# Kernel optimization log

Hardware: AMD Instinct MI355X
Metric: run time of the kernel (lower is better)

## Reference

```python
import jax, jax.numpy as jnp
import numpy as np

H = 128; TIME_DIM = 8; LAM = 0.01; NUM_LAYERS = 2; B = 64
N_FACT = 100000; N_COMP = 5000; E = 500000; D_FACT = 384; D_COMP = 64
MLP_IN = 2 + 2 * (TIME_DIM // 2) + 1  # 11


def setup_inputs() -> dict:
    key = jax.random.key(0)
    ks = jax.random.split(key, 40)
    rn = lambda k, sh, s=0.05: jax.random.normal(k, sh, jnp.float32) * s
    inp = {
        'x_fact': jax.random.normal(ks[0], (N_FACT, D_FACT), jnp.float32),
        'x_comp': jax.random.normal(ks[1], (N_COMP, D_COMP), jnp.float32),
        'ea_f2c': jax.random.uniform(ks[2], (E, 2), jnp.float32),
        'ea_c2f': jax.random.uniform(ks[3], (E, 2), jnp.float32),
        'ei_f2c_src': jax.random.randint(ks[4], (E,), 0, N_FACT, jnp.int32),
        'ei_f2c_dst': jax.random.randint(ks[5], (E,), 0, N_COMP, jnp.int32),
        'ei_c2f_src': jax.random.randint(ks[6], (E,), 0, N_COMP, jnp.int32),
        'ei_c2f_dst': jax.random.randint(ks[7], (E,), 0, N_FACT, jnp.int32),
        'fact_batch': jnp.sort(jax.random.randint(ks[8], (N_FACT,), 0, B, jnp.int32)),
        'comp_batch': jnp.sort(jax.random.randint(ks[9], (N_COMP,), 0, B, jnp.int32)),
        # lazy per-type input projections
        'W_in_fact': rn(ks[10], (D_FACT, H)), 'b_in_fact': jnp.zeros((H,), jnp.float32),
        'W_in_comp': rn(ks[11], (D_COMP, H)), 'b_in_comp': jnp.zeros((H,), jnp.float32),
        # EdgeAttrEncoder MLP: 11 -> 32 -> 16 -> 1
        'eW1': rn(ks[12], (MLP_IN, 32)), 'eb1': jnp.zeros((32,), jnp.float32),
        'eW2': rn(ks[13], (32, 16)), 'eb2': jnp.zeros((16,), jnp.float32),
        'eW3': rn(ks[14], (16, 1)), 'eb3': jnp.zeros((1,), jnp.float32),
        # GraphConv per layer (axis0) per edge type (axis1: 0=f->c, 1=c->f)
        'W_rel': rn(ks[15], (NUM_LAYERS, 2, H, H)), 'b_rel': jnp.zeros((NUM_LAYERS, 2, H), jnp.float32),
        'W_root': rn(ks[16], (NUM_LAYERS, 2, H, H)),
        # shared post LayerNorm per node type (axis0: 0=fact, 1=company)
        'ln_scale': jnp.ones((2, H), jnp.float32), 'ln_bias': jnp.zeros((2, H), jnp.float32),
        # classifier 2H -> H -> 1
        'Wc1': rn(ks[17], (2 * H, H)), 'bc1': jnp.zeros((H,), jnp.float32),
        'Wc2': rn(ks[18], (H, 1)), 'bc2': jnp.zeros((1,), jnp.float32),
    }
    return inp


def _edge_gate(ea, eW1, eb1, eW2, eb2, eW3, eb3):
    # ea: [E,2] -> gate [E]
    sent = jnp.clip(ea[:, 0:1], -1.0, 1.0)
    decay = ea[:, 1:2]
    # decay in [0,1] -> delta_t = -log(decay)/lambda, clamped >= 0
    dt = jnp.maximum(-jnp.log(jnp.clip(decay, 1e-6, None)) / LAM, 0.0)
    ds = jnp.clip(dt / 30.0, 0.0, 12.0)
    freqs = jnp.arange(1, TIME_DIM // 2 + 1, dtype=ds.dtype)
    tvec = jnp.concatenate([jnp.sin(ds * freqs), jnp.cos(ds * freqs), ds], axis=-1)
    x = jnp.concatenate([sent, jnp.log1p(dt), tvec], axis=-1)  # [E,11]
    h = jax.nn.relu(x @ eW1 + eb1)
    h = jax.nn.relu(h @ eW2 + eb2)
    return jax.nn.sigmoid(h @ eW3 + eb3)[:, 0]


def _layernorm(x, scale, bias, eps=1e-5):
    mu = jnp.mean(x, axis=-1, keepdims=True)
    var = jnp.var(x, axis=-1, keepdims=True)
    return (x - mu) * jax.lax.rsqrt(var + eps) * scale + bias


def _seg_mean(x, seg, n):
    s = jax.ops.segment_sum(x, seg, num_segments=n)
    c = jax.ops.segment_sum(jnp.ones((x.shape[0], 1), x.dtype), seg, num_segments=n)
    return s / jnp.maximum(c, 1.0)


def reference(x_fact, x_comp, ea_f2c, ea_c2f, ei_f2c_src, ei_f2c_dst, ei_c2f_src,
              ei_c2f_dst, fact_batch, comp_batch, W_in_fact, b_in_fact, W_in_comp,
              b_in_comp, eW1, eb1, eW2, eb2, eW3, eb3, W_rel, b_rel, W_root,
              ln_scale, ln_bias, Wc1, bc1, Wc2, bc2):
    # per-type input projection + ReLU
    xf = jax.nn.relu(x_fact @ W_in_fact + b_in_fact)   # [N_fact, H]
    xc = jax.nn.relu(x_comp @ W_in_comp + b_in_comp)   # [N_comp, H]
    # MLP-gated edge weights (shared encoder across relations)
    w_f2c = _edge_gate(ea_f2c, eW1, eb1, eW2, eb2, eW3, eb3)  # [E]
    w_c2f = _edge_gate(ea_c2f, eW1, eb1, eW2, eb2, eW3, eb3)  # [E]
    nf, nc = xf.shape[0], xc.shape[0]
    for l in range(NUM_LAYERS):
        prev_f, prev_c = xf, xc
        # GraphConv: lin_rel(sum_j w_ij * x_j) + lin_root(x_i)  (aggr='add')
        agg_c = jax.ops.segment_sum(xf[ei_f2c_src] * w_f2c[:, None], ei_f2c_dst, num_segments=nc)
        new_c = agg_c @ W_rel[l, 0] + b_rel[l, 0] + xc @ W_root[l, 0]
        agg_f = jax.ops.segment_sum(xc[ei_c2f_src] * w_c2f[:, None], ei_c2f_dst, num_segments=nf)
        new_f = agg_f @ W_rel[l, 1] + b_rel[l, 1] + xf @ W_root[l, 1]
        # ReLU -> residual -> shared per-type LayerNorm
        xf = _layernorm(jax.nn.relu(new_f) + prev_f, ln_scale[0], ln_bias[0])
        xc = _layernorm(jax.nn.relu(new_c) + prev_c, ln_scale[1], ln_bias[1])
    fact_pool = _seg_mean(xf, fact_batch, B)   # [B, H]
    comp_pool = _seg_mean(xc, comp_batch, B)   # [B, H]
    pooled = jnp.concatenate([fact_pool, comp_pool], axis=-1)  # [B, 2H]
    h = jax.nn.relu(pooled @ Wc1 + bc1)
    return (h @ Wc2 + bc2)[:, 0]  # [B] logits
```

## Files before the change

### kernel.cpp

```cpp
#include <hip/hip_runtime.h>
#include <math.h>

#define H 128
#define EDGES 500000
#define NFACT 100000
#define NCOMP 5000
#define BATCH 64
#define NTILE 6250

typedef _Float16 half8_t __attribute__((ext_vector_type(8)));
typedef float floatx4 __attribute__((ext_vector_type(4)));

__device__ inline short4 f4_to_h4(float4 v){
  union { short4 s; _Float16 h[4]; } u;
  u.h[0]=(_Float16)v.x; u.h[1]=(_Float16)v.y; u.h[2]=(_Float16)v.z; u.h[3]=(_Float16)v.w;
  return u.s;
}

__global__ __launch_bounds__(1024) void k_scan1(const int* __restrict__ cnt, int n,
                                                int* __restrict__ offs, int* __restrict__ part){
  __shared__ int sh[1024];
  int tid = threadIdx.x;
  int i = blockIdx.x*1024 + tid;
  int v = (i < n) ? cnt[i] : 0;
  sh[tid] = v;
  __syncthreads();
  for (int d = 1; d < 1024; d <<= 1){
    int t = (tid >= d) ? sh[tid-d] : 0;
    __syncthreads();
    sh[tid] += t;
    __syncthreads();
  }
  if (i < n) offs[i] = sh[tid] - v;
  if (tid == 1023) part[blockIdx.x] = sh[1023];
}

__global__ void k_scan2(int* part, int nb){
  __shared__ int sh[128];
  int tid = threadIdx.x;
  int v = (tid < nb) ? part[tid] : 0;
  sh[tid] = v;
  __syncthreads();
  for (int d = 1; d < 128; d <<= 1){
    int t = (tid >= d) ? sh[tid-d] : 0;
    __syncthreads();
    sh[tid] += t;
    __syncthreads();
  }
  if (tid < nb) part[tid] = sh[tid] - v;
}

__global__ __launch_bounds__(1024) void k_scan3(int* offs, int n, const int* __restrict__ part, int total){
  int i = blockIdx.x*1024 + threadIdx.x;
  if (i < n) offs[i] += part[blockIdx.x];
  if (i == 0) offs[n] = total;
}

__global__ void k_fill2d(const int* __restrict__ src0, const int* __restrict__ dst0,
                         const float* __restrict__ w0, const int* __restrict__ offs0,
                         int* __restrict__ cur0, int4* __restrict__ ed0,
                         const int* __restrict__ src1, const int* __restrict__ dst1,
                         const float* __restrict__ w1, const int* __restrict__ offs1,
                         int* __restrict__ cur1, int4* __restrict__ ed1, int n){
  int half = gridDim.x >> 1;
  int dir = blockIdx.x >= half;
  const int* src = dir ? src1 : src0;
  const int* dst = dir ? dst1 : dst0;
  const float* w = dir ? w1 : w0;
  const int* offs = dir ? offs1 : offs0;
  int* cur = dir ? cur1 : cur0;
  int4* ed = dir ? ed1 : ed0;
  int bid = blockIdx.x - (dir ? half : 0);
  for (int e = bid*blockDim.x + threadIdx.x; e < n; e += half*blockDim.x){
    int d = dst[e];
    int p = offs[d] + atomicAdd(&cur[d], 1);
    ed[p] = make_int4(src[e], __float_as_int(w[e]), d, 0);
  }
}

__global__ __launch_bounds__(256) void k_prep(const float* __restrict__ W_in,
                                              const float* __restrict__ W_rel,
                                              const float* __restrict__ W_root,
                                              _Float16* __restrict__ wt_in,
                                              _Float16* __restrict__ wcat0,
                                              _Float16* __restrict__ wcat1){
  int i = blockIdx.x*256 + threadIdx.x;
  if (i < 49152){
    int n = i / 384, k = i % 384;
    wt_in[i] = (_Float16)W_in[k*128 + n];
  } else if (i < 49152 + 32768){
    int j = i - 49152;
    int n = j / 256, k = j % 256;
    const float* Wr = W_rel  + 1*16384;
    const float* Wo = W_root + 1*16384;
    wcat0[j] = (_Float16)(k < 128 ? Wr[k*128+n] : Wo[(k-128)*128+n]);
  } else if (i < 49152 + 65536){
    int j = i - 49152 - 32768;
    int n = j / 256, k = j % 256;
    const float* Wr = W_rel  + 3*16384;
    const float* Wo = W_root + 3*16384;
    wcat1[j] = (_Float16)(k < 128 ? Wr[k*128+n] : Wo[(k-128)*128+n]);
  }
}

__global__ __launch_bounds__(256) void k_gate2(const float* __restrict__ ea0,
                       const float* __restrict__ ea1,
                       const int* __restrict__ dst0, const int* __restrict__ dst1,
                       int* __restrict__ cnt0, int* __restrict__ cnt1,
                       const float* __restrict__ eW1, const float* __restrict__ eb1,
                       const float* __restrict__ eW2, const float* __restrict__ eb2,
                       const float* __restrict__ eW3, const float* __restrict__ eb3,
                       float* __restrict__ wout0, float* __restrict__ wout1, int n){
  __shared__ float w1t[32*12];
  __shared__ float w2s[32*16];
  __shared__ float b1s[32], b2s[16], w3s[16];
  __shared__ float b3s;
  int tid = threadIdx.x;
  for (int i = tid; i < 352; i += 256){
    int k = i >> 5, c = i & 31;
    w1t[c*12 + k] = eW1[i];
  }
  if (tid < 32) w1t[tid*12 + 11] = 0.f;
  for (int i = tid; i < 512; i += 256) w2s[i] = eW2[i];
  if (tid < 32) b1s[tid] = eb1[tid];
  if (tid < 16) b2s[tid] = eb2[tid];
  if (tid < 16) w3s[tid] = eW3[tid];
  if (tid == 0) b3s = eb3[0];
  __syncthreads();

  int half = gridDim.x >> 1;
  int dir = blockIdx.x >= half;
  const float* ea = dir ? ea1 : ea0;
  const int* dst  = dir ? dst1 : dst0;
  int* cnt        = dir ? cnt1 : cnt0;
  float* wout     = dir ? wout1 : wout0;
  int bid = blockIdx.x - (dir ? half : 0);

  const float4* w1t4 = (const float4*)w1t;
  const float4* w24  = (const float4*)w2s;
  float4 b2v0 = ((const float4*)b2s)[0], b2v1 = ((const float4*)b2s)[1];
  float4 b2v2 = ((const float4*)b2s)[2], b2v3 = ((const float4*)b2s)[3];
  float4 w3v0 = ((const float4*)w3s)[0], w3v1 = ((const float4*)w3s)[1];
  float4 w3v2 = ((const float4*)w3s)[2], w3v3 = ((const float4*)w3s)[3];

  for (int e = bid*blockDim.x + tid; e < n; e += half*blockDim.x){
    float2 eav = ((const float2*)ea)[e];
    float sent  = fminf(fmaxf(eav.x, -1.f), 1.f);
    float decay = eav.y;
    float dt = fmaxf(-__logf(fmaxf(decay, 1e-6f)) * 100.f, 0.f);
    float ds = fminf(dt * (1.f/30.f), 12.f);
    float s1 = __sinf(ds), c1 = __cosf(ds);
    float s2v = 2.f*s1*c1;
    float c2v = 1.f - 2.f*s1*s1;
    float s3v = s1*c2v + c1*s2v;
    float c3v = c1*c2v - s1*s2v;
    float s4v = 2.f*s2v*c2v;
    float c4v = 1.f - 2.f*s2v*s2v;
    float4 x0 = make_float4(sent, __logf(1.f + dt), s1, s2v);
    float4 x1 = make_float4(s3v, s4v, c1, c2v);
    float4 x2 = make_float4(c3v, c4v, ds, 0.f);

    float4 sa = b2v0, sb = b2v1, sc = b2v2, sd = b2v3;
    #pragma unroll 2
    for (int i = 0; i < 32; i++){
      float4 wa = w1t4[i*3+0], wb = w1t4[i*3+1], wc = w1t4[i*3+2];
      float h = b1s[i];
      h += x0.x*wa.x + x0.y*wa.y + x0.z*wa.z + x0.w*wa.w;
      h += x1.x*wb.x + x1.y*wb.y + x1.z*wb.z + x1.w*wb.w;
      h += x2.x*wc.x + x2.y*wc.y + x2.z*wc.z;
      h = fmaxf(h, 0.f);
      float4 va = w24[i*4+0], vb = w24[i*4+1], vc = w24[i*4+2], vd = w24[i*4+3];
      sa.x += h*va.x; sa.y += h*va.y; sa.z += h*va.z; sa.w += h*va.w;
      sb.x += h*vb.x; sb.y += h*vb.y; sb.z += h*vb.z; sb.w += h*vb.w;
      sc.x += h*vc.x; sc.y += h*vc.y; sc.z += h*vc.z; sc.w += h*vc.w;
      sd.x += h*vd.x; sd.y += h*vd.y; sd.z += h*vd.z; sd.w += h*vd.w;
    }
    float o = b3s;
    o += fmaxf(sa.x,0.f)*w3v0.x + fmaxf(sa.y,0.f)*w3v0.y + fmaxf(sa.z,0.f)*w3v0.z + fmaxf(sa.w,0.f)*w3v0.w;
    o += fmaxf(sb.x,0.f)*w3v1.x + fmaxf(sb.y,0.f)*w3v1.y + fmaxf(sb.z,0.f)*w3v1.z + fmaxf(sb.w,0.f)*w3v1.w;
    o += fmaxf(sc.x,0.f)*w3v2.x + fmaxf(sc.y,0.f)*w3v2.y + fmaxf(sc.z,0.f)*w3v2.z + fmaxf(sc.w,0.f)*w3v2.w;
    o += fmaxf(sd.x,0.f)*w3v3.x + fmaxf(sd.y,0.f)*w3v3.y + fmaxf(sd.z,0.f)*w3v3.z + fmaxf(sd.w,0.f)*w3v3.w;
    wout[e] = __fdividef(1.f, 1.f + __expf(-o));
    atomicAdd(&cnt[dst[e]], 1);
  }
}

template<int K, int R>
__global__ __launch_bounds__(128) void k_input_s(const float* __restrict__ X, const float* __restrict__ W,
                                                 const float* __restrict__ bias, float* __restrict__ Y){
  __shared__ float xs[R*K];
  int t = threadIdx.x;
  long row0 = (long)blockIdx.x * R;
  const float4* src = (const float4*)(X + row0*K);
  float4* d4 = (float4*)xs;
  for (int i = t; i < R*K/4; i += 128) d4[i] = src[i];
  __syncthreads();
  float acc[R];
  #pragma unroll
  for (int r = 0; r < R; r++) acc[r] = 0.f;
  for (int k4 = 0; k4 < K/4; k4++){
    int kb = k4*4;
    float w0 = W[(kb+0)*H+t], w1 = W[(kb+1)*H+t], w2 = W[(kb+2)*H+t], w3 = W[(kb+3)*H+t];
    #pragma unroll
    for (int r = 0; r < R; r++){
      float4 xv = ((const float4*)(xs + r*K))[k4];
      acc[r] += xv.x*w0 + xv.y*w1 + xv.z*w2 + xv.w*w3;
    }
  }
  float b = bias[t];
  #pragma unroll
  for (int r = 0; r < R; r++)
    Y[(row0+r)*H + t] = fmaxf(acc[r] + b, 0.f);
}

__global__ __launch_bounds__(256, 2) void k_input_m(const float* __restrict__ X,
                                                 const _Float16* __restrict__ Wt,
                                                 const float* __restrict__ bias,
                                                 float* __restrict__ Y){
  __shared__ _Float16 xs[16][392];
  __shared__ float tb[4*16*36];
  int t = threadIdx.x;
  int lane = t & 63, wv = t >> 6;
  int m = lane & 15, q = lane >> 4;

  half8_t wreg[2][12];
  float bcol[2];
  #pragma unroll
  for (int j = 0; j < 2; j++){
    int col = (wv*2 + j)*16 + m;
    const _Float16* wb = Wt + (size_t)col*384 + q*8;
    #pragma unroll
    for (int ks = 0; ks < 12; ks++) wreg[j][ks] = *(const half8_t*)(wb + ks*32);
    bcol[j] = bias[col];
  }

  int row_i[6], c4_i[6];
  #pragma unroll
  for (int i = 0; i < 6; i++){
    int idx = i*256 + t;
    row_i[i] = idx/96; c4_i[i] = idx - row_i[i]*96;
  }

  int tpb = (NTILE + gridDim.x - 1)/gridDim.x;
  int tb0 = blockIdx.x*tpb, tb1 = tb0 + tpb;
  if (tb1 > NTILE) tb1 = NTILE;
  if (tb0 >= tb1) return;

  const float4* X4 = (const float4*)X;
  float4 r[6];
  #pragma unroll
  for (int i = 0; i < 6; i++) r[i] = X4[(size_t)tb0*1536 + i*256 + t];

  float* tbw = &tb[wv*576];
  int rowl = lane >> 2, c8l = lane & 3;

  for (int tile = tb0; tile < tb1; ++tile){
    __syncthreads();
    #pragma unroll
    for (int i = 0; i < 6; i++)
      *(short4*)&xs[row_i[i]][c4_i[i]*4] = f4_to_h4(r[i]);
    __syncthreads();
    if (tile + 1 < tb1){
      size_t base = (size_t)(tile+1)*1536;
      #pragma unroll
      for (int i = 0; i < 6; i++) r[i] = X4[base + i*256 + t];
    }
    __builtin_amdgcn_sched_barrier(0);

    floatx4 acc0 = (floatx4){0.f,0.f,0.f,0.f};
    floatx4 acc1 = (floatx4){0.f,0.f,0.f,0.f};
    #pragma unroll
    for (int ks = 0; ks < 12; ks++){
      half8_t av = *(const half8_t*)&xs[m][ks*32 + q*8];
      acc0 = __builtin_amdgcn_mfma_f32_16x16x32_f16(av, wreg[0][ks], acc0, 0, 0, 0);
      acc1 = __builtin_amdgcn_mfma_f32_16x16x32_f16(av, wreg[1][ks], acc1, 0, 0, 0);
    }
    long rb = (long)tile*16;
    #pragma unroll
    for (int j = 0; j < 2; j++){
      floatx4 a = j ? acc1 : acc0;
      int lc = j*16 + m;
      #pragma unroll
      for (int i2 = 0; i2 < 4; i2++)
        tbw[(q*4+i2)*36 + lc] = fmaxf(a[i2] + bcol[j], 0.f);
    }
    __syncthreads();
    {
      const float* srcp = tbw + rowl*36 + c8l*8;
      float* dstp = Y + (rb + rowl)*H + wv*32 + c8l*8;
      *(float4*)dstp       = *(const float4*)(srcp);
      *(float4*)(dstp + 4) = *(const float4*)(srcp + 4);
    }
  }
}

__global__ __launch_bounds__(256) void k_layer_m(
    const float* __restrict__ xsrc, const float* __restrict__ xprev,
    const int* __restrict__ offs, const int4* __restrict__ ed,
    const _Float16* __restrict__ Wt, const float* __restrict__ brel,
    const float* __restrict__ lnsc, const float* __restrict__ lnbi,
    float* __restrict__ xnext){
  __shared__ float tball[4*2304];
  int t = threadIdx.x;
  int lane = t & 63, wv = t >> 6;
  long tile = (long)blockIdx.x*4 + wv;
  if (tile*16 >= NFACT) return;
  long row0 = tile*16;
  float* tb = tball + wv*2304;
  _Float16 (*xin)[264] = reinterpret_cast<_Float16 (*)[264]>(tb);
  int c = lane & 31, g = lane >> 5;
  int grow0 = g*8;
  #pragma unroll
  for (int j = 0; j < 8; j++){
    int lr = grow0 + j;
    ((short4*)&xin[lr][0])[c] = make_short4(0,0,0,0);
    float4 pv = ((const float4*)(xprev + (row0+lr)*H))[c];
    ((short4*)&xin[lr][128])[c] = f4_to_h4(pv);
  }
  int lo = offs[row0 + grow0], hi = offs[row0 + grow0 + 8];
  float4 a = make_float4(0.f,0.f,0.f,0.f);
  int cur = (int)row0 + grow0;
  int idx = lo;
  int nb = (hi - lo) >> 3;
  int4 rec[8];
  if (nb > 0){
    #pragma unroll
    for (int j = 0; j < 8; j++) rec[j] = ed[idx+j];
  }
  for (int b = 0; b < nb; b++){
    int nxt = idx + 8;
    int4 rec2[8];
    if (b + 1 < nb){
      #pragma unroll
      for (int j = 0; j < 8; j++) rec2[j] = ed[nxt+j];
    }
    float4 v[8];
    #pragma unroll
    for (int j = 0; j < 8; j++) v[j] = ((const float4*)(xsrc + (long)rec[j].x*H))[c];
    #pragma unroll
    for (int j = 0; j < 8; j++){
      float w = __int_as_float(rec[j].y);
      if (rec[j].z != cur){ ((short4*)&xin[cur-(int)row0][0])[c] = f4_to_h4(a); a = make_float4(0.f,0.f,0.f,0.f); cur = rec[j].z; }
      a.x += v[j].x*w; a.y += v[j].y*w; a.z += v[j].z*w; a.w += v[j].w*w;
    }
    #pragma unroll
    for (int j = 0; j < 8; j++) rec[j] = rec2[j];
    idx = nxt;
  }
  for (; idx < hi; idx++){
    int4 mrec = ed[idx];
    float4 v = ((const float4*)(xsrc + (long)mrec.x*H))[c];
    float w = __int_as_float(mrec.y);
    if (mrec.z != cur){ ((short4*)&xin[cur-(int)row0][0])[c] = f4_to_h4(a); a = make_float4(0.f,0.f,0.f,0.f); cur = mrec.z; }
    a.x += v.x*w; a.y += v.y*w; a.z += v.z*w; a.w += v.w*w;
  }
  if (lo < hi) ((short4*)&xin[cur-(int)row0][0])[c] = f4_to_h4(a);

  int m = lane & 15, q = lane >> 4;
  floatx4 acc[8];
  #pragma unroll
  for (int nt = 0; nt < 8; nt++) acc[nt] = (floatx4){0.f,0.f,0.f,0.f};
  #pragma unroll
  for (int ks = 0; ks < 8; ks++){
    half8_t av = *(const half8_t*)&xin[m][ks*32 + q*8];
    #pragma unroll
    for (int nt = 0; nt < 8; nt++){
      half8_t bv = *(const half8_t*)(Wt + (size_t)(nt*16 + m)*256 + ks*32 + q*8);
      acc[nt] = __builtin_amdgcn_mfma_f32_16x16x32_f16(av, bv, acc[nt], 0, 0, 0);
    }
  }
  float vs[8][4];
  float s[4] = {0.f,0.f,0.f,0.f}, ss[4] = {0.f,0.f,0.f,0.f};
  #pragma unroll
  for (int nt = 0; nt < 8; nt++){
    int col = nt*16 + m;
    float b = brel[col];
    #pragma unroll
    for (int i = 0; i < 4; i++){
      int lr = q*4 + i;
      float pv = (float)xin[lr][128 + col];
      float v = fmaxf(acc[nt][i] + b, 0.f) + pv;
      vs[nt][i] = v;
      s[i] += v; ss[i] += v*v;
    }
  }
  #pragma unroll
  for (int i = 0; i < 4; i++){
    #pragma unroll
    for (int mm = 1; mm < 16; mm <<= 1){
      s[i]  += __shfl_xor(s[i],  mm, 64);
      ss[i] += __shfl_xor(ss[i], mm, 64);
    }
  }
  asm volatile("" ::: "memory");
  #pragma unroll
  for (int nt = 0; nt < 8; nt++){
    int col = nt*16 + m;
    float lsc = lnsc[col], lbi = lnbi[col];
    int chnk = col >> 5, lc = col & 31;
    #pragma unroll
    for (int i = 0; i < 4; i++){
      float mu  = s[i]*(1.f/H);
      float var = ss[i]*(1.f/H) - mu*mu;
      float rstd = rsqrtf(var + 1e-5f);
      tb[(q*4+i)*144 + chnk*36 + lc] = (vs[nt][i] - mu)*rstd*lsc + lbi;
    }
  }
  asm volatile("" ::: "memory");
  {
    int rowl = lane >> 2, c8 = lane & 3;
    const float* srcp = &tb[rowl*144 + c8*36];
    float4* dst4 = (float4*)(xnext + (row0 + rowl)*H + c8*32);
    #pragma unroll
    for (int k = 0; k < 8; k++)
      dst4[k] = *(const float4*)(srcp + k*4);
  }
}

template<int R>
__global__ __launch_bounds__(128) void k_layer(
    const float* __restrict__ xsrc, const float* __restrict__ xprev,
    const int* __restrict__ offs, const int4* __restrict__ ed,
    const float* __restrict__ Wrel, const float* __restrict__ brel,
    const float* __restrict__ Wroot, const float* __restrict__ lnsc,
    const float* __restrict__ lnbi, float* __restrict__ xnext){
  constexpr int RG = R/4;
  __shared__ float xin[R][256];
  int t = threadIdx.x, c = t & 31, g = t >> 5;
  long row0 = (long)blockIdx.x * R;
  int grow0 = g*RG;
  #pragma unroll
  for (int j = 0; j < RG; j++){
    int lr = grow0 + j;
    ((float4*)&xin[lr][0])[c] = make_float4(0.f,0.f,0.f,0.f);
    ((float4*)&xin[lr][128])[c] = ((const float4*)(xprev + (row0+lr)*H))[c];
  }
  int lo = offs[row0 + grow0], hi = offs[row0 + grow0 + RG];
  float4 a = make_float4(0.f,0.f,0.f,0.f);
  int cur = (int)row0 + grow0;
  int idx = lo;
  for (; idx + 8 <= hi; idx += 8){
    int4 m[8];
    #pragma unroll
    for (int j = 0; j < 8; j++) m[j] = ed[idx+j];
    float4 v[8];
    #pragma unroll
    for (int j = 0; j < 8; j++) v[j] = ((const float4*)(xsrc + (long)m[j].x*H))[c];
    #pragma unroll
    for (int j = 0; j < 8; j++){
      float w = __int_as_float(m[j].y);
      if (m[j].z != cur){ ((float4*)&xin[cur-(int)row0][0])[c] = a; a = make_float4(0.f,0.f,0.f,0.f); cur = m[j].z; }
      a.x += v[j].x*w; a.y += v[j].y*w; a.z += v[j].z*w; a.w += v[j].w*w;
    }
  }
  for (; idx < hi; idx++){
    int4 m = ed[idx];
    float4 v = ((const float4*)(xsrc + (long)m.x*H))[c];
    float w = __int_as_float(m.y);
    if (m.z != cur){ ((float4*)&xin[cur-(int)row0][0])[c] = a; a = make_float4(0.f,0.f,0.f,0.f); cur = m.z; }
    a.x += v.x*w; a.y += v.y*w; a.z += v.z*w; a.w += v.w*w;
  }
  if (lo < hi) ((float4*)&xin[cur-(int)row0][0])[c] = a;

  float4 acc[RG];
  float4 bv = ((const float4*)brel)[c];
  #pragma unroll
  for (int j = 0; j < RG; j++) acc[j] = bv;
  #pragma unroll
  for (int p = 0; p < 2; p++){
    const float4* Wp = (const float4*)(p ? Wroot : Wrel) + c;
    #pragma unroll 4
    for (int k4 = 0; k4 < 32; k4++){
      float4 xv[RG];
      #pragma unroll
      for (int j = 0; j < RG; j++)
        xv[j] = ((const float4*)xin[grow0+j])[p*32 + k4];
      #pragma unroll
      for (int kk = 0; kk < 4; kk++){
        float4 wv = Wp[(size_t)(k4*4+kk)*32];
        #pragma unroll
        for (int j = 0; j < RG; j++){
          float xk = (kk==0) ? xv[j].x : (kk==1) ? xv[j].y : (kk==2) ? xv[j].z : xv[j].w;
          acc[j].x += xk*wv.x; acc[j].y += xk*wv.y; acc[j].z += xk*wv.z; acc[j].w += xk*wv.w;
        }
      }
    }
  }
  float4 lsc = ((const float4*)lnsc)[c];
  float4 lbi = ((const float4*)lnbi)[c];
  #pragma unroll
  for (int j = 0; j < RG; j++){
    int lr = grow0 + j;
    float4 pv = ((const float4*)&xin[lr][128])[c];
    float4 v;
    v.x = fmaxf(acc[j].x, 0.f) + pv.x;
    v.y = fmaxf(acc[j].y, 0.f) + pv.y;
    v.z = fmaxf(acc[j].z, 0.f) + pv.z;
    v.w = fmaxf(acc[j].w, 0.f) + pv.w;
    float s  = v.x + v.y + v.z + v.w;
    float ss = v.x*v.x + v.y*v.y + v.z*v.z + v.w*v.w;
    #pragma unroll
    for (int mm = 1; mm < 32; mm <<= 1){ s += __shfl_xor(s, mm, 64); ss += __shfl_xor(ss, mm, 64); }
    float mu  = s*(1.f/H);
    float var = ss*(1.f/H) - mu*mu;
    float rstd = rsqrtf(var + 1e-5f);
    float4 o;
    o.x = (v.x - mu)*rstd*lsc.x + lbi.x;
    o.y = (v.y - mu)*rstd*lsc.y + lbi.y;
    o.z = (v.z - mu)*rstd*lsc.z + lbi.z;
    o.w = (v.w - mu)*rstd*lsc.w + lbi.w;
    ((float4*)(xnext + (row0+lr)*H))[c] = o;
  }
}

#define PCHUNK 128
#define FBLK ((NFACT + PCHUNK - 1) / PCHUNK)
#define CBLK ((NCOMP + PCHUNK - 1) / PCHUNK)

__global__ __launch_bounds__(128) void k_pool_acc(const float* __restrict__ xf, const float* __restrict__ xc,
                                                  const int* __restrict__ fb, const int* __restrict__ cb,
                                                  float* __restrict__ pooled){
  int t = threadIdx.x;
  int b = blockIdx.x;
  if (b < FBLK){
    int start = b*PCHUNK, end = start + PCHUNK; if (end > NFACT) end = NFACT;
    float s = 0.f; int curb = -1;
    for (int i = start; i < end; i++){
      int bb = fb[i];
      if (bb != curb){
        if (curb >= 0) atomicAdd(&pooled[curb*256 + t], s);
        curb = bb; s = 0.f;
      }
      s += xf[(long)i*H + t];
    }
    if (curb >= 0) atomicAdd(&pooled[curb*256 + t], s);
  } else {
    int bbk = b - FBLK;
    int start = bbk*PCHUNK, end = start + PCHUNK; if (end > NCOMP) end = NCOMP;
    float s = 0.f; int curb = -1;
    for (int i = start; i < end; i++){
      int bb = cb[i];
      if (bb != curb){
        if (curb >= 0) atomicAdd(&pooled[curb*256 + 128 + t], s);
        curb = bb; s = 0.f;
      }
      s += xc[(long)i*H + t];
    }
    if (curb >= 0) atomicAdd(&pooled[curb*256 + 128 + t], s);
  }
}

__device__ inline int lowerb(const int* a, int n, int key){
  int lo = 0, hi = n;
  while (lo < hi){ int m = (lo+hi) >> 1; if (a[m] < key) lo = m+1; else hi = m; }
  return lo;
}

__global__ __launch_bounds__(128) void k_head(const float* __restrict__ pooled,
                                              const int* __restrict__ fb, const int* __restrict__ cb,
                                              const float* __restrict__ Wc1, const float* __restrict__ bc1,
                                              const float* __restrict__ Wc2, const float* __restrict__ bc2,
                                              float* __restrict__ out){
  __shared__ float p[256];
  __shared__ float red[2];
  int t = threadIdx.x, b = blockIdx.x;
  int flo = lowerb(fb, NFACT, b), fhi = lowerb(fb, NFACT, b+1);
  int clo = lowerb(cb, NCOMP, b), chi = lowerb(cb, NCOMP, b+1);
  float fc = (float)((fhi - flo) > 1 ? (fhi - flo) : 1);
  float cc = (float)((chi - clo) > 1 ? (chi - clo) : 1);
  p[t]       = pooled[b*256 + t] / fc;
  p[128 + t] = pooled[b*256 + 128 + t] / cc;
  __syncthreads();
  float acc = bc1[t];
  #pragma unroll 4
  for (int k = 0; k < 256; k++) acc += p[k]*Wc1[k*H + t];
  float h = fmaxf(acc, 0.f)*Wc2[t];
  #pragma unroll
  for (int m = 1; m < 64; m <<= 1) h += __shfl_xor(h, m, 64);
  if ((t & 63) == 0) red[t>>6] = h;
  __syncthreads();
  if (t == 0) out[b] = red[0] + red[1] + bc2[0];
}

extern "C" void kernel_launch(void* const* d_in, const int* in_sizes, int n_in,
                              void* d_out, int out_size, void* d_ws, size_t ws_size,
                              hipStream_t stream){
  const float* x_fact = (const float*)d_in[0];
  const float* x_comp = (const float*)d_in[1];
  const float* ea_f2c = (const float*)d_in[2];
  const float* ea_c2f = (const float*)d_in[3];
  const int* s_f2c   = (const int*)d_in[4];
  const int* dst_f2c = (const int*)d_in[5];
  const int* s_c2f   = (const int*)d_in[6];
  const int* dst_c2f = (const int*)d_in[7];
  const int* fb = (const int*)d_in[8];
  const int* cb = (const int*)d_in[9];
  const float* W_in_f = (const float*)d_in[10];
  const float* b_in_f = (const float*)d_in[11];
  const float* W_in_c = (const float*)d_in[12];
  const float* b_in_c = (const float*)d_in[13];
  const float* eW1 = (const float*)d_in[14]; const float* eb1 = (const float*)d_in[15];
  const float* eW2 = (const float*)d_in[16]; const float* eb2 = (const float*)d_in[17];
  const float* eW3 = (const float*)d_in[18]; const float* eb3 = (const float*)d_in[19];
  const float* W_rel = (const float*)d_in[20]; const float* b_rel = (const float*)d_in[21];
  const float* W_root = (const float*)d_in[22];
  const float* ln_s = (const float*)d_in[23]; const float* ln_b = (const float*)d_in[24];
  const float* Wc1 = (const float*)d_in[25]; const float* bc1 = (const float*)d_in[26];
  const float* Wc2 = (const float*)d_in[27]; const float* bc2 = (const float*)d_in[28];
  float* out = (float*)d_out;

  char* ws = (char*)d_ws;
  size_t off = 0;
  auto alloc = [&](size_t bytes)->char*{ char* p = ws + off; off = (off + bytes + 255) & ~(size_t)255; return p; };
  float* xf0   = (float*)alloc((size_t)NFACT*H*4);
  float* xf1   = (float*)alloc((size_t)NFACT*H*4);
  float* xc0   = (float*)alloc((size_t)NCOMP*H*4);
  float* xc1   = (float*)alloc((size_t)NCOMP*H*4);
  float* w_f2c = (float*)alloc((size_t)EDGES*4);
  float* w_c2f = (float*)alloc((size_t)EDGES*4);
  int4* ed_f2c = (int4*)alloc((size_t)EDGES*16);
  int4* ed_c2f = (int4*)alloc((size_t)EDGES*16);
  int* off_f2c = (int*)alloc((size_t)(NCOMP+1)*4);
  int* cur_f2c = (int*)alloc((size_t)NCOMP*4);
  int* off_c2f = (int*)alloc((size_t)(NFACT+1)*4);
  int* cur_c2f = (int*)alloc((size_t)NFACT*4);
  int* part    = (int*)alloc(128*4);
  float* pooled= (float*)alloc((size_t)BATCH*256*4);
  _Float16* wt_in = (_Float16*)alloc((size_t)49152*2);
  _Float16* wcat0 = (_Float16*)alloc((size_t)32768*2);
  _Float16* wcat1 = (_Float16*)alloc((size_t)32768*2);

  k_prep<<<448,256,0,stream>>>(W_in_f, W_rel, W_root, wt_in, wcat0, wcat1);
  hipMemsetAsync(cur_f2c, 0, NCOMP*4, stream);
  hipMemsetAsync(cur_c2f, 0, NFACT*4, stream);
  k_gate2<<<1024,256,0,stream>>>(ea_f2c, ea_c2f, dst_f2c, dst_c2f,
                                 cur_f2c, cur_c2f,
                                 eW1,eb1,eW2,eb2,eW3,eb3, w_f2c, w_c2f, EDGES);

  {
    int nb = (NCOMP + 1023)/1024;
    k_scan1<<<nb,1024,0,stream>>>(cur_f2c, NCOMP, off_f2c, part);
    k_scan2<<<1,128,0,stream>>>(part, nb);
    k_scan3<<<nb,1024,0,stream>>>(off_f2c, NCOMP, part, EDGES);
  }
  {
    int nb = (NFACT + 1023)/1024;
    k_scan1<<<nb,1024,0,stream>>>(cur_c2f, NFACT, off_c2f, part);
    k_scan2<<<1,128,0,stream>>>(part, nb);
    k_scan3<<<nb,1024,0,stream>>>(off_c2f, NFACT, part, EDGES);
  }
  hipMemsetAsync(cur_f2c, 0, NCOMP*4, stream);
  hipMemsetAsync(cur_c2f, 0, NFACT*4, stream);
  k_fill2d<<<1024,256,0,stream>>>(s_f2c, dst_f2c, w_f2c, off_f2c, cur_f2c, ed_f2c,
                                  s_c2f, dst_c2f, w_c2f, off_c2f, cur_c2f, ed_c2f, EDGES);

  k_input_m<<<512,256,0,stream>>>(x_fact, wt_in, b_in_f, xf0);
  k_input_s<64,8><<<NCOMP/8,128,0,stream>>>(x_comp, W_in_c, b_in_c, xc0);

  const float* xf_p = xf0; const float* xc_p = xc0;
  float* xf_n = xf1; float* xc_n = xc1;
  for (int l = 0; l < 2; l++){
    const float* Wr0 = W_rel  + (size_t)(l*2+0)*H*H;
    const float* br0 = b_rel  + (size_t)(l*2+0)*H;
    const float* br1 = b_rel  + (size_t)(l*2+1)*H;
    const float* Wo0 = W_root + (size_t)(l*2+0)*H*H;
    const _Float16* wcat = (l == 0) ? wcat0 : wcat1;
    k_layer<4><<<NCOMP/4,128,0,stream>>>(xf_p, xc_p, off_f2c, ed_f2c,
                                         Wr0, br0, Wo0, ln_s + H, ln_b + H, xc_n);
    k_layer_m<<<(NTILE+3)/4,256,0,stream>>>(xc_p, xf_p, off_c2f, ed_c2f,
                                            wcat, br1, ln_s, ln_b, xf_n);
    const float* tf = xf_p; xf_p = xf_n; xf_n = (float*)tf;
    const float* tc = xc_p; xc_p = xc_n; xc_n = (float*)tc;
  }

  hipMemsetAsync(pooled, 0, (size_t)BATCH*256*4, stream);
  k_pool_acc<<<FBLK + CBLK,128,0,stream>>>(xf_p, xc_p, fb, cb, pooled);
  k_head<<<BATCH,128,0,stream>>>(pooled, fb, cb, Wc1, bc1, Wc2, bc2, out);
}
```

Measured before the change: 803.6 us.

## Fuse company and fact GraphConv layer kernels into one launch

Replaces the two per-layer kernels (company update and fact update) with a single launch. Block index selects the branch: the first blocks run the MFMA fact path and the rest run the scalar company path, two 4-row tiles per 256-thread block. Since both updates read only the previous layer's state, the latency-bound company gathers (about 100 edges per row) can overlap with the fact work instead of running serially, and one launch is saved per layer. In exchange, every block now reserves the larger shared-memory buffer, and the fact branch loses its software prefetch of the next batch of edge records, which may raise gather latency.

```diff
diff --git a/kernel.cpp b/kernel.cpp
--- a/kernel.cpp
+++ b/kernel.cpp
@@ -7,6 +7,8 @@
 #define NCOMP 5000
 #define BATCH 64
 #define NTILE 6250
+#define NFB 1563
+#define NCB 625
 
 typedef _Float16 half8_t __attribute__((ext_vector_type(8)));
 typedef float floatx4 __attribute__((ext_vector_type(4)));
@@ -294,222 +296,196 @@
   }
 }
 
-__global__ __launch_bounds__(256) void k_layer_m(
-    const float* __restrict__ xsrc, const float* __restrict__ xprev,
-    const int* __restrict__ offs, const int4* __restrict__ ed,
-    const _Float16* __restrict__ Wt, const float* __restrict__ brel,
-    const float* __restrict__ lnsc, const float* __restrict__ lnbi,
-    float* __restrict__ xnext){
-  __shared__ float tball[4*2304];
+__global__ __launch_bounds__(256) void k_layer_fused(
+    const float* __restrict__ xf_p, const float* __restrict__ xc_p,
+    const int* __restrict__ offs_c, const int4* __restrict__ ed_c,
+    const float* __restrict__ Wrel, const float* __restrict__ brc,
+    const float* __restrict__ Wroot,
+    const float* __restrict__ lnsC, const float* __restrict__ lnbC,
+    float* __restrict__ xc_n,
+    const int* __restrict__ offs_f, const int4* __restrict__ ed_f,
+    const _Float16* __restrict__ Wt, const float* __restrict__ brf,
+    const float* __restrict__ lnsF, const float* __restrict__ lnbF,
+    float* __restrict__ xf_n){
+  __shared__ __align__(16) float smemf[9216];
   int t = threadIdx.x;
-  int lane = t & 63, wv = t >> 6;
-  long tile = (long)blockIdx.x*4 + wv;
-  if (tile*16 >= NFACT) return;
-  long row0 = tile*16;
-  float* tb = tball + wv*2304;
-  _Float16 (*xin)[264] = reinterpret_cast<_Float16 (*)[264]>(tb);
-  int c = lane & 31, g = lane >> 5;
-  int grow0 = g*8;
-  #pragma unroll
-  for (int j = 0; j < 8; j++){
-    int lr = grow0 + j;
-    ((short4*)&xin[lr][0])[c] = make_short4(0,0,0,0);
-    float4 pv = ((const float4*)(xprev + (row0+lr)*H))[c];
-    ((short4*)&xin[lr][128])[c] = f4_to_h4(pv);
-  }
-  int lo = offs[row0 + grow0], hi = offs[row0 + grow0 + 8];
-  float4 a = make_float4(0.f,0.f,0.f,0.f);
-  int cur = (int)row0 + grow0;
-  int idx = lo;
-  int nb = (hi - lo) >> 3;
-  int4 rec[8];
-  if (nb > 0){
-    #pragma unroll
-    for (int j = 0; j < 8; j++) rec[j] = ed[idx+j];
-  }
-  for (int b = 0; b < nb; b++){
-    int nxt = idx + 8;
-    int4 rec2[8];
-    if (b + 1 < nb){
-      #pragma unroll
-      for (int j = 0; j < 8; j++) rec2[j] = ed[nxt+j];
-    }
-    float4 v[8];
-    #pragma unroll
-    for (int j = 0; j < 8; j++) v[j] = ((const float4*)(xsrc + (long)rec[j].x*H))[c];
+  if ((int)blockIdx.x < NFB){
+    int lane = t & 63, wv = t >> 6;
+    long tile = (long)blockIdx.x*4 + wv;
+    if (tile >= NTILE) return;
+    long row0 = tile*16;
+    float* tb = smemf + wv*2304;
+    _Float16 (*xin)[264] = reinterpret_cast<_Float16 (*)[264]>(tb);
+    int c = lane & 31, g = lane >> 5;
+    int grow0 = g*8;
     #pragma unroll
     for (int j = 0; j < 8; j++){
-      float w = __int_as_float(rec[j].y);
-      if (rec[j].z != cur){ ((short4*)&xin[cur-(int)row0][0])[c] = f4_to_h4(a); a = make_float4(0.f,0.f,0.f,0.f); cur = rec[j].z; }
-      a.x += v[j].x*w; a.y += v[j].y*w; a.z += v[j].z*w; a.w += v[j].w*w;
-    }
-    #pragma unroll
-    for (int j = 0; j < 8; j++) rec[j] = rec2[j];
-    idx = nxt;
-  }
-  for (; idx < hi; idx++){
-    int4 mrec = ed[idx];
-    float4 v = ((const float4*)(xsrc + (long)mrec.x*H))[c];
-    float w = __int_as_float(mrec.y);
-    if (mrec.z != cur){ ((short4*)&xin[cur-(int)row0][0])[c] = f4_to_h4(a); a = make_float4(0.f,0.f,0.f,0.f); cur = mrec.z; }
-    a.x += v.x*w; a.y += v.y*w; a.z += v.z*w; a.w += v.w*w;
-  }
-  if (lo < hi) ((short4*)&xin[cur-(int)row0][0])[c] = f4_to_h4(a);
-
-  int m = lane & 15, q = lane >> 4;
-  floatx4 acc[8];
-  #pragma unroll
-  for (int nt = 0; nt < 8; nt++) acc[nt] = (floatx4){0.f,0.f,0.f,0.f};
-  #pragma unroll
-  for (int ks = 0; ks < 8; ks++){
-    half8_t av = *(const half8_t*)&xin[m][ks*32 + q*8];
+      int lr = grow0 + j;
+      ((short4*)&xin[lr][0])[c] = make_short4(0,0,0,0);
+      float4 pv = ((const float4*)(xf_p + (row0+lr)*H))[c];
+      ((short4*)&xin[lr][128])[c] = f4_to_h4(pv);
+    }
+    int lo = offs_f[row0 + grow0], hi = offs_f[row0 + grow0 + 8];
+    float4 a = make_float4(0.f,0.f,0.f,0.f);
+    int cur = (int)row0 + grow0;
+    int idx = lo;
+    for (; idx + 8 <= hi; idx += 8){
+      int4 rec[8];
+      #pragma unroll
+      for (int j = 0; j < 8; j++) rec[j] = ed_f[idx+j];
+      float4 v[8];
+      #pragma unroll
+      for (int j = 0; j < 8; j++) v[j] = ((const float4*)(xc_p + (long)rec[j].x*H))[c];
+      #pragma unroll
+      for (int j = 0; j < 8; j++){
+        float w = __int_as_float(rec[j].y);
+        if (rec[j].z != cur){ ((short4*)&xin[cur-(int)row0][0])[c] = f4_to_h4(a); a = make_float4(0.f,0.f,0.f,0.f); cur = rec[j].z; }
+        a.x += v[j].x*w; a.y += v[j].y*w; a.z += v[j].z*w; a.w += v[j].w*w;
+      }
+    }
+    for (; idx < hi; idx++){
+      int4 rec = ed_f[idx];
+      float4 v = ((const float4*)(xc_p + (long)rec.x*H))[c];
+      float w = __int_as_float(rec.y);
+      if (rec.z != cur){ ((short4*)&xin[cur-(int)row0][0])[c] = f4_to_h4(a); a = make_float4(0.f,0.f,0.f,0.f); cur = rec.z; }
+      a.x += v.x*w; a.y += v.y*w; a.z += v.z*w; a.w += v.w*w;
+    }
+    if (lo < hi) ((short4*)&xin[cur-(int)row0][0])[c] = f4_to_h4(a);
+
+    int m = lane & 15, q = lane >> 4;
+    floatx4 acc[8];
+    #pragma unroll
+    for (int nt = 0; nt < 8; nt++) acc[nt] = (floatx4){0.f,0.f,0.f,0.f};
+    #pragma unroll
+    for (int ks = 0; ks < 8; ks++){
+      half8_t av = *(const half8_t*)&xin[m][ks*32 + q*8];
+      #pragma unroll
+      for (int nt = 0; nt < 8; nt++){
+        half8_t bv = *(const half8_t*)(Wt + (size_t)(nt*16 + m)*256 + ks*32 + q*8);
+        acc[nt] = __builtin_amdgcn_mfma_f32_16x16x32_f16(av, bv, acc[nt], 0, 0, 0);
+      }
+    }
+    float vs[8][4];
+    float s[4] = {0.f,0.f,0.f,0.f}, ss[4] = {0.f,0.f,0.f,0.f};
     #pragma unroll
     for (int nt = 0; nt < 8; nt++){
-      half8_t bv = *(const half8_t*)(Wt + (size_t)(nt*16 + m)*256 + ks*32 + q*8);
-      acc[nt] = __builtin_amdgcn_mfma_f32_16x16x32_f16(av, bv, acc[nt], 0, 0, 0);
-    }
-  }
-  float vs[8][4];
-  float s[4] = {0.f,0.f,0.f,0.f}, ss[4] = {0.f,0.f,0.f,0.f};
-  #pragma unroll
-  for (int nt = 0; nt < 8; nt++){
-    int col = nt*16 + m;
-    float b = brel[col];
+      int col = nt*16 + m;
+      float b = brf[col];
+      #pragma unroll
+      for (int i = 0; i < 4; i++){
+        int lr = q*4 + i;
+        float pv = (float)xin[lr][128 + col];
+        float v = fmaxf(acc[nt][i] + b, 0.f) + pv;
+        vs[nt][i] = v;
+        s[i] += v; ss[i] += v*v;
+      }
+    }
     #pragma unroll
     for (int i = 0; i < 4; i++){
-      int lr = q*4 + i;
-      float pv = (float)xin[lr][128 + col];
-      float v = fmaxf(acc[nt][i] + b, 0.f) + pv;
-      vs[nt][i] = v;
-      s[i] += v; ss[i] += v*v;
-    }
-  }
-  #pragma unroll
-  for (int i = 0; i < 4; i++){
-    #pragma unroll
-    for (int mm = 1; mm < 16; mm <<= 1){
-      s[i]  += __shfl_xor(s[i],  mm, 64);
-      ss[i] += __shfl_xor(ss[i], mm, 64);
-    }
-  }
-  asm volatile("" ::: "memory");
-  #pragma unroll
-  for (int nt = 0; nt < 8; nt++){
-    int col = nt*16 + m;
-    float lsc = lnsc[col], lbi = lnbi[col];
-    int chnk = col >> 5, lc = col & 31;
-    #pragma unroll
-    for (int i = 0; i < 4; i++){
-      float mu  = s[i]*(1.f/H);
-      float var = ss[i]*(1.f/H) - mu*mu;
+      #pragma unroll
+      for (int mm = 1; mm < 16; mm <<= 1){
+        s[i]  += __shfl_xor(s[i],  mm, 64);
+        ss[i] += __shfl_xor(ss[i], mm, 64);
+      }
+    }
+    asm volatile("" ::: "memory");
+    #pragma unroll
+    for (int nt = 0; nt < 8; nt++){
+      int col = nt*16 + m;
+      float lsc = lnsF[col], lbi = lnbF[col];
+      int chnk = col >> 5, lc = col & 31;
+      #pragma unroll
+      for (int i = 0; i < 4; i++){
+        float mu  = s[i]*(1.f/H);
+        float var = ss[i]*(1.f/H) - mu*mu;
+        float rstd = rsqrtf(var + 1e-5f);
+        tb[(q*4+i)*144 + chnk*36 + lc] = (vs[nt][i] - mu)*rstd*lsc + lbi;
+      }
+    }
+    asm volatile("" ::: "memory");
+    {
+      int rowl = lane >> 2, c8 = lane & 3;
+      const float* srcp = &tb[rowl*144 + c8*36];
+      float4* dst4 = (float4*)(xf_n + (row0 + rowl)*H + c8*32);
+      #pragma unroll
+      for (int k = 0; k < 8; k++)
+        dst4[k] = *(const float4*)(srcp + k*4);
+    }
+  } else {
+    int unit = t >> 7, tt = t & 127;
+    int ctile = ((int)blockIdx.x - NFB)*2 + unit;
+    float (*xin)[256] = (float(*)[256])(smemf + unit*1024);
+    int c = tt & 31, g = tt >> 5;
+    long row0 = (long)ctile * 4;
+    {
+      ((float4*)&xin[g][0])[c] = make_float4(0.f,0.f,0.f,0.f);
+      ((float4*)&xin[g][128])[c] = ((const float4*)(xc_p + (row0+g)*H))[c];
+    }
+    int lo = offs_c[row0 + g], hi = offs_c[row0 + g + 1];
+    float4 a = make_float4(0.f,0.f,0.f,0.f);
+    int cur = (int)row0 + g;
+    int idx = lo;
+    for (; idx + 8 <= hi; idx += 8){
+      int4 rec[8];
+      #pragma unroll
+      for (int j = 0; j < 8; j++) rec[j] = ed_c[idx+j];
+      float4 v[8];
+      #pragma unroll
+      for (int j = 0; j < 8; j++) v[j] = ((const float4*)(xf_p + (long)rec[j].x*H))[c];
+      #pragma unroll
+      for (int j = 0; j < 8; j++){
+        float w = __int_as_float(rec[j].y);
+        if (rec[j].z != cur){ ((float4*)&xin[cur-(int)row0][0])[c] = a; a = make_float4(0.f,0.f,0.f,0.f); cur = rec[j].z; }
+        a.x += v[j].x*w; a.y += v[j].y*w; a.z += v[j].z*w; a.w += v[j].w*w;
+      }
+    }
+    for (; idx < hi; idx++){
+      int4 rec = ed_c[idx];
+      float4 v = ((const float4*)(xf_p + (long)rec.x*H))[c];
+      float w = __int_as_float(rec.y);
+      if (rec.z != cur){ ((float4*)&xin[cur-(int)row0][0])[c] = a; a = make_float4(0.f,0.f,0.f,0.f); cur = rec.z; }
+      a.x += v.x*w; a.y += v.y*w; a.z += v.z*w; a.w += v.w*w;
+    }
+    if (lo < hi) ((float4*)&xin[cur-(int)row0][0])[c] = a;
+
+    float4 acc = ((const float4*)brc)[c];
+    #pragma unroll
+    for (int p = 0; p < 2; p++){
+      const float4* Wp = (const float4*)(p ? Wroot : Wrel) + c;
+      #pragma unroll 4
+      for (int k4 = 0; k4 < 32; k4++){
+        float4 xv = ((const float4*)xin[g])[p*32 + k4];
+        #pragma unroll
+        for (int kk = 0; kk < 4; kk++){
+          float4 wv = Wp[(size_t)(k4*4+kk)*32];
+          float xk = (kk==0) ? xv.x : (kk==1) ? xv.y : (kk==2) ? xv.z : xv.w;
+          acc.x += xk*wv.x; acc.y += xk*wv.y; acc.z += xk*wv.z; acc.w += xk*wv.w;
+        }
+      }
+    }
+    float4 lsc = ((const float4*)lnsC)[c];
+    float4 lbi = ((const float4*)lnbC)[c];
+    {
+      float4 pv = ((const float4*)&xin[g][128])[c];
+      float4 v;
+      v.x = fmaxf(acc.x, 0.f) + pv.x;
+      v.y = fmaxf(acc.y, 0.f) + pv.y;
+      v.z = fmaxf(acc.z, 0.f) + pv.z;
+      v.w = fmaxf(acc.w, 0.f) + pv.w;
+      float s  = v.x + v.y + v.z + v.w;
+      float ss = v.x*v.x + v.y*v.y + v.z*v.z + v.w*v.w;
+      #pragma unroll
+      for (int mm = 1; mm < 32; mm <<= 1){ s += __shfl_xor(s, mm, 64); ss += __shfl_xor(ss, mm, 64); }
+      float mu  = s*(1.f/H);
+      float var = ss*(1.f/H) - mu*mu;
       float rstd = rsqrtf(var + 1e-5f);
-      tb[(q*4+i)*144 + chnk*36 + lc] = (vs[nt][i] - mu)*rstd*lsc + lbi;
-    }
-  }
-  asm volatile("" ::: "memory");
-  {
-    int rowl = lane >> 2, c8 = lane & 3;
-    const float* srcp = &tb[rowl*144 + c8*36];
-    float4* dst4 = (float4*)(xnext + (row0 + rowl)*H + c8*32);
-    #pragma unroll
-    for (int k = 0; k < 8; k++)
-      dst4[k] = *(const float4*)(srcp + k*4);
-  }
-}
-
-template<int R>
-__global__ __launch_bounds__(128) void k_layer(
-    const float* __restrict__ xsrc, const float* __restrict__ xprev,
-    const int* __restrict__ offs, const int4* __restrict__ ed,
-    const float* __restrict__ Wrel, const float* __restrict__ brel,
-    const float* __restrict__ Wroot, const float* __restrict__ lnsc,
-    const float* __restrict__ lnbi, float* __restrict__ xnext){
-  constexpr int RG = R/4;
-  __shared__ float xin[R][256];
-  int t = threadIdx.x, c = t & 31, g = t >> 5;
-  long row0 = (long)blockIdx.x * R;
-  int grow0 = g*RG;
-  #pragma unroll
-  for (int j = 0; j < RG; j++){
-    int lr = grow0 + j;
-    ((float4*)&xin[lr][0])[c] = make_float4(0.f,0.f,0.f,0.f);
-    ((float4*)&xin[lr][128])[c] = ((const float4*)(xprev + (row0+lr)*H))[c];
-  }
-  int lo = offs[row0 + grow0], hi = offs[row0 + grow0 + RG];
-  float4 a = make_float4(0.f,0.f,0.f,0.f);
-  int cur = (int)row0 + grow0;
-  int idx = lo;
-  for (; idx + 8 <= hi; idx += 8){
-    int4 m[8];
-    #pragma unroll
-    for (int j = 0; j < 8; j++) m[j] = ed[idx+j];
-    float4 v[8];
-    #pragma unroll
-    for (int j = 0; j < 8; j++) v[j] = ((const float4*)(xsrc + (long)m[j].x*H))[c];
-    #pragma unroll
-    for (int j = 0; j < 8; j++){
-      float w = __int_as_float(m[j].y);
-      if (m[j].z != cur){ ((float4*)&xin[cur-(int)row0][0])[c] = a; a = make_float4(0.f,0.f,0.f,0.f); cur = m[j].z; }
-      a.x += v[j].x*w; a.y += v[j].y*w; a.z += v[j].z*w; a.w += v[j].w*w;
-    }
-  }
-  for (; idx < hi; idx++){
-    int4 m = ed[idx];
-    float4 v = ((const float4*)(xsrc + (long)m.x*H))[c];
-    float w = __int_as_float(m.y);
-    if (m.z != cur){ ((float4*)&xin[cur-(int)row0][0])[c] = a; a = make_float4(0.f,0.f,0.f,0.f); cur = m.z; }
-    a.x += v.x*w; a.y += v.y*w; a.z += v.z*w; a.w += v.w*w;
-  }
-  if (lo < hi) ((float4*)&xin[cur-(int)row0][0])[c] = a;
-
-  float4 acc[RG];
-  float4 bv = ((const float4*)brel)[c];
-  #pragma unroll
-  for (int j = 0; j < RG; j++) acc[j] = bv;
-  #pragma unroll
-  for (int p = 0; p < 2; p++){
-    const float4* Wp = (const float4*)(p ? Wroot : Wrel) + c;
-    #pragma unroll 4
-    for (int k4 = 0; k4 < 32; k4++){
-      float4 xv[RG];
-      #pragma unroll
-      for (int j = 0; j < RG; j++)
-        xv[j] = ((const float4*)xin[grow0+j])[p*32 + k4];
-      #pragma unroll
-      for (int kk = 0; kk < 4; kk++){
-        float4 wv = Wp[(size_t)(k4*4+kk)*32];
-        #pragma unroll
-        for (int j = 0; j < RG; j++){
-          float xk = (kk==0) ? xv[j].x : (kk==1) ? xv[j].y : (kk==2) ? xv[j].z : xv[j].w;
-          acc[j].x += xk*wv.x; acc[j].y += xk*wv.y; acc[j].z += xk*wv.z; acc[j].w += xk*wv.w;
-        }
-      }
-    }
-  }
-  float4 lsc = ((const float4*)lnsc)[c];
-  float4 lbi = ((const float4*)lnbi)[c];
-  #pragma unroll
-  for (int j = 0; j < RG; j++){
-    int lr = grow0 + j;
-    float4 pv = ((const float4*)&xin[lr][128])[c];
-    float4 v;
-    v.x = fmaxf(acc[j].x, 0.f) + pv.x;
-    v.y = fmaxf(acc[j].y, 0.f) + pv.y;
-    v.z = fmaxf(acc[j].z, 0.f) + pv.z;
-    v.w = fmaxf(acc[j].w, 0.f) + pv.w;
-    float s  = v.x + v.y + v.z + v.w;
-    float ss = v.x*v.x + v.y*v.y + v.z*v.z + v.w*v.w;
-    #pragma unroll
-    for (int mm = 1; mm < 32; mm <<= 1){ s += __shfl_xor(s, mm, 64); ss += __shfl_xor(ss, mm, 64); }
-    float mu  = s*(1.f/H);
-    float var = ss*(1.f/H) - mu*mu;
-    float rstd = rsqrtf(var + 1e-5f);
-    float4 o;
-    o.x = (v.x - mu)*rstd*lsc.x + lbi.x;
-    o.y = (v.y - mu)*rstd*lsc.y + lbi.y;
-    o.z = (v.z - mu)*rstd*lsc.z + lbi.z;
-    o.w = (v.w - mu)*rstd*lsc.w + lbi.w;
-    ((float4*)(xnext + (row0+lr)*H))[c] = o;
+      float4 o;
+      o.x = (v.x - mu)*rstd*lsc.x + lbi.x;
+      o.y = (v.y - mu)*rstd*lsc.y + lbi.y;
+      o.z = (v.z - mu)*rstd*lsc.z + lbi.z;
+      o.w = (v.w - mu)*rstd*lsc.w + lbi.w;
+      ((float4*)(xc_n + (row0+g)*H))[c] = o;
+    }
   }
 }
 
@@ -665,10 +641,9 @@
     const float* br1 = b_rel  + (size_t)(l*2+1)*H;
     const float* Wo0 = W_root + (size_t)(l*2+0)*H*H;
     const _Float16* wcat = (l == 0) ? wcat0 : wcat1;
-    k_layer<4><<<NCOMP/4,128,0,stream>>>(xf_p, xc_p, off_f2c, ed_f2c,
-                                         Wr0, br0, Wo0, ln_s + H, ln_b + H, xc_n);
-    k_layer_m<<<(NTILE+3)/4,256,0,stream>>>(xc_p, xf_p, off_c2f, ed_c2f,
-                                            wcat, br1, ln_s, ln_b, xf_n);
+    k_layer_fused<<<NFB + NCB,256,0,stream>>>(
+        xf_p, xc_p, off_f2c, ed_f2c, Wr0, br0, Wo0, ln_s + H, ln_b + H, xc_n,
+        off_c2f, ed_c2f, wcat, br1, ln_s, ln_b, xf_n);
     const float* tf = xf_p; xf_p = xf_n; xf_n = (float*)tf;
     const float* tc = xc_p; xc_p = xc_n; xc_n = (float*)tc;
   }
```

Result: faster. 775.0 us (-3.6%).
